# Optimization experiments

Measured on AMD Instinct MI355X. Metric: run time of the kernel, lower is better.

The kernel has to match this reference:

```python
import jax, jax.numpy as jnp
import numpy as np

EMBED_DIM = 256
NUM_HEADS = 8
HEAD_DIM = EMBED_DIM // NUM_HEADS


def setup_inputs() -> dict:
    key = jax.random.key(0)
    ks = jax.random.split(key, 16)
    B, N, E = 4, 2048, EMBED_DIM
    s = 1.0 / np.sqrt(E)
    inp = {
        "x": jax.random.normal(ks[0], (B, N, E), jnp.float32),
        "influence_matrix": jax.random.uniform(ks[1], (B, N, N), jnp.float32),
        "Wq": jax.random.normal(ks[2], (E, E), jnp.float32) * s,
        "Wk": jax.random.normal(ks[3], (E, E), jnp.float32) * s,
        "Wv": jax.random.normal(ks[4], (E, E), jnp.float32) * s,
        "Wo": jax.random.normal(ks[5], (E, E), jnp.float32) * s,
        "bo": jnp.zeros((E,), jnp.float32),
        "iw1": jnp.array(1.0, jnp.float32),
        "ib1": jnp.array(0.0, jnp.float32),
        "iw2": jnp.array(1.0, jnp.float32),
        "ib2": jnp.array(0.0, jnp.float32),
        "W1": jax.random.normal(ks[6], (E, E), jnp.float32) * s,
        "b1": jnp.zeros((E,), jnp.float32),
        "W2": jax.random.normal(ks[7], (E, E), jnp.float32) * s,
        "b2": jnp.zeros((E,), jnp.float32),
        "g1": jnp.ones((E,), jnp.float32),
        "beta1": jnp.zeros((E,), jnp.float32),
        "g2": jnp.ones((E,), jnp.float32),
        "beta2": jnp.zeros((E,), jnp.float32),
    }
    return inp


def _layer_norm(x, g, b, eps=1e-5):
    mu = jnp.mean(x, axis=-1, keepdims=True)
    var = jnp.var(x, axis=-1, keepdims=True)
    return (x - mu) * jax.lax.rsqrt(var + eps) * g + b


def _attention(x, infl, Wq, Wk, Wv, Wo, bo, iw1, ib1, iw2, ib2):
    B, N, E = x.shape
    H, D = NUM_HEADS, HEAD_DIM
    # torch nn.Linear: y = x @ W.T ; here W is stored as (E, E) used directly.
    q = (x @ Wq).reshape(B, N, H, D)
    k = (x @ Wk).reshape(B, N, H, D)
    v = (x @ Wv).reshape(B, N, H, D)
    scores = jnp.einsum("bqhd,bkhd->bhqk", q, k) / np.sqrt(D)  # [B,H,N,N]
    scores = scores + (iw1 * infl + ib1)[:, None, :, :]
    w = jax.nn.softmax(scores, axis=-1)
    w = w * (iw2 * infl + ib2)[:, None, :, :]
    out = jnp.einsum("bhqk,bkhd->bqhd", w, v).reshape(B, N, E)
    return out @ Wo + bo


def reference(x, influence_matrix, Wq, Wk, Wv, Wo, bo, iw1, ib1, iw2, ib2,
              W1, b1, W2, b2, g1, beta1, g2, beta2):
    h = _attention(_layer_norm(x, g1, beta1), influence_matrix,
                   Wq, Wk, Wv, Wo, bo, iw1, ib1, iw2, ib2) + x
    ffn = jax.nn.relu(_layer_norm(h, g2, beta2) @ W1 + b1) @ W2 + b2
    return ffn + h
```

## Files before the change

### kernel.cpp

```cpp
#include <hip/hip_runtime.h>
#include <hip/hip_bf16.h>

#define B_  4
#define N_  2048
#define E_  256
#define H_  8
#define D_  32
#define QT  32
#define KC  64
#define HPB 4
#define VTP 72
#define PP  72
#define IFP 68
#define LOG2E 1.4426950408889634f

typedef __attribute__((ext_vector_type(8))) short bfx8;
typedef __attribute__((ext_vector_type(4))) float fx4;

__device__ __forceinline__ unsigned short f2bf(float f) {
    unsigned int u = __float_as_uint(f);
    u += 0x7fffu + ((u >> 16) & 1u);
    return (unsigned short)(u >> 16);
}

__global__ __launch_bounds__(256) void prep_w(
    const float* Wa, const float* Wb, const float* Wc,
    const float* Wd, const float* We, const float* Wf,
    unsigned short* Oa, unsigned short* Ob, unsigned short* Oc,
    unsigned short* Od, unsigned short* Oe, unsigned short* Of)
{
    int z = blockIdx.z;
    const float* src = z == 0 ? Wa : z == 1 ? Wb : z == 2 ? Wc
                     : z == 3 ? Wd : z == 4 ? We : Wf;
    unsigned short* dst = z == 0 ? Oa : z == 1 ? Ob : z == 2 ? Oc
                        : z == 3 ? Od : z == 4 ? Oe : Of;
    __shared__ float t[32][33];
    int n0 = blockIdx.x * 32, k0 = blockIdx.y * 32;
    int tx = threadIdx.x & 31, ty = threadIdx.x >> 5;
#pragma unroll
    for (int i = 0; i < 4; i++)
        t[ty + i * 8][tx] = src[(k0 + ty + i * 8) * E_ + n0 + tx];
    __syncthreads();
#pragma unroll
    for (int i = 0; i < 4; i++)
        dst[(n0 + ty + i * 8) * E_ + k0 + tx] = f2bf(t[tx][ty + i * 8]);
}

__global__ __launch_bounds__(256) void ln_kernel(const float* __restrict__ x,
                                                 const float* __restrict__ g,
                                                 const float* __restrict__ be,
                                                 unsigned short* __restrict__ out)
{
    long row = blockIdx.x;
    int t = threadIdx.x;
    float v = x[row * E_ + t];
    float s = v, s2 = v * v;
#pragma unroll
    for (int off = 32; off; off >>= 1) {
        s  += __shfl_xor(s,  off, 64);
        s2 += __shfl_xor(s2, off, 64);
    }
    __shared__ float rs[4], rs2[4];
    int w = t >> 6;
    if ((t & 63) == 0) { rs[w] = s; rs2[w] = s2; }
    __syncthreads();
    s  = rs[0] + rs[1] + rs[2] + rs[3];
    s2 = rs2[0] + rs2[1] + rs2[2] + rs2[3];
    float mu  = s * (1.0f / E_);
    float var = s2 * (1.0f / E_) - mu * mu;
    float rstd = rsqrtf(var + 1e-5f);
    out[row * E_ + t] = f2bf((v - mu) * rstd * g[t] + be[t]);
}

__device__ __forceinline__ void gemm_core(
    const unsigned short* __restrict__ A,
    const unsigned short* __restrict__ Wt,
    const float* __restrict__ bias,
    const float* __restrict__ resid,
    void* __restrict__ Cv, int relu, int obf, int m0, int n0)
{
    __shared__ unsigned short As[64 * 264];
    __shared__ unsigned short Bs[64 * 264];
    int tid = threadIdx.x;

    {
        const unsigned short* Ab = A  + (long)m0 * E_;
        const unsigned short* Bb = Wt + (long)n0 * E_;
        bfx8 va[8], vb[8];
#pragma unroll
        for (int i = 0; i < 8; i++) va[i] = *(const bfx8*)&Ab[(i * 256 + tid) * 8];
#pragma unroll
        for (int i = 0; i < 8; i++) vb[i] = *(const bfx8*)&Bb[(i * 256 + tid) * 8];
#pragma unroll
        for (int i = 0; i < 8; i++) {
            int fo = i * 256 + tid;
            int row = fo >> 5, c8 = fo & 31;
            *(bfx8*)&As[row * 264 + c8 * 8] = va[i];
            *(bfx8*)&Bs[row * 264 + c8 * 8] = vb[i];
        }
    }
    __syncthreads();

    int lane = tid & 63, w = tid >> 6;
    int c = lane & 15, g = lane >> 4;
    int wm = (w >> 1) * 32, wn = (w & 1) * 32;
    fx4 acc[2][2] = {};

#pragma unroll
    for (int ks = 0; ks < 8; ks++) {
        bfx8 a0 = *(const bfx8*)&As[(wm + c)      * 264 + ks * 32 + g * 8];
        bfx8 a1 = *(const bfx8*)&As[(wm + 16 + c) * 264 + ks * 32 + g * 8];
        bfx8 b0 = *(const bfx8*)&Bs[(wn + c)      * 264 + ks * 32 + g * 8];
        bfx8 b1 = *(const bfx8*)&Bs[(wn + 16 + c) * 264 + ks * 32 + g * 8];
        acc[0][0] = __builtin_amdgcn_mfma_f32_16x16x32_bf16(a0, b0, acc[0][0], 0, 0, 0);
        acc[0][1] = __builtin_amdgcn_mfma_f32_16x16x32_bf16(a0, b1, acc[0][1], 0, 0, 0);
        acc[1][0] = __builtin_amdgcn_mfma_f32_16x16x32_bf16(a1, b0, acc[1][0], 0, 0, 0);
        acc[1][1] = __builtin_amdgcn_mfma_f32_16x16x32_bf16(a1, b1, acc[1][1], 0, 0, 0);
    }

#pragma unroll
    for (int fm = 0; fm < 2; fm++)
#pragma unroll
        for (int r = 0; r < 4; r++) {
            int m = m0 + wm + fm * 16 + g * 4 + r;
#pragma unroll
            for (int fn = 0; fn < 2; fn++) {
                int n = n0 + wn + fn * 16 + c;
                float o = acc[fm][fn][r];
                if (bias)  o += bias[n];
                if (relu)  o = fmaxf(o, 0.f);
                if (resid) o += resid[(long)m * E_ + n];
                if (obf) ((unsigned short*)Cv)[(long)m * E_ + n] = f2bf(o);
                else     ((float*)Cv)[(long)m * E_ + n] = o;
            }
        }
}

__global__ __launch_bounds__(256, 2) void gemm_mfma(
    const unsigned short* __restrict__ A,
    const unsigned short* __restrict__ Wt,
    const float* __restrict__ bias,
    const float* __restrict__ resid,
    void* __restrict__ Cv, int relu, int obf)
{
    gemm_core(A, Wt, bias, resid, Cv, relu, obf, blockIdx.x * 64, blockIdx.y * 64);
}

__global__ __launch_bounds__(256, 2) void gemm_qkv(
    const unsigned short* __restrict__ A,
    const unsigned short* __restrict__ Wq, unsigned short* __restrict__ qo,
    const unsigned short* __restrict__ Wk, unsigned short* __restrict__ ko,
    const unsigned short* __restrict__ Wv, unsigned short* __restrict__ vo)
{
    int z = blockIdx.z;
    const unsigned short* Wt = z == 0 ? Wq : z == 1 ? Wk : Wv;
    unsigned short*       Cv = z == 0 ? qo : z == 1 ? ko : vo;
    gemm_core(A, Wt, nullptr, nullptr, Cv, 0, 1, blockIdx.x * 64, blockIdx.y * 64);
}

__global__ __launch_bounds__(256, 2) void attn_mfma(
    const unsigned short* __restrict__ q,
    const unsigned short* __restrict__ k,
    const unsigned short* __restrict__ v,
    const float* __restrict__ infl,
    const float* __restrict__ iw1p, const float* __restrict__ ib1p,
    const float* __restrict__ iw2p, const float* __restrict__ ib2p,
    unsigned short* __restrict__ out)
{
    const int bx  = blockIdx.x;
    const int xcd = bx & 7;
    const int b   = xcd >> 1;
    const int hg  = (xcd & 1) * HPB;
    const int q0  = (bx >> 3) * QT;
    const int tid = threadIdx.x;
    const int h    = tid >> 6;
    const int head = hg + h;
    const int lane = tid & 63;
    const int c = lane & 15, g = lane >> 4, g4 = g * 4;

    const float iw1e = iw1p[0] * LOG2E, ib1e = ib1p[0] * LOG2E;
    const float iw2 = iw2p[0], ib2 = ib2p[0];
    const float scale2 = 0.17677669529663687f * LOG2E;
    const float cadd = ib1e - 16.0f * LOG2E;

    __shared__ unsigned short vt_lds[HPB][D_][VTP];
    __shared__ unsigned short p_lds[HPB][QT][PP];
    __shared__ unsigned short infl_lds[2][QT][IFP];

    bfx8 qf0 = *(const bfx8*)&q[((long)(b * N_ + q0 +      c)) * E_ + head * D_ + g * 8];
    bfx8 qf1 = *(const bfx8*)&q[((long)(b * N_ + q0 + 16 + c)) * E_ + head * D_ + g * 8];

    const unsigned short* kbase = &k[((long)(b * N_) + c) * E_ + head * D_ + g * 8];
    const int p2 = lane & 31, dh = (lane >> 5) * 16;
    const unsigned short* vbase = &v[((long)(b * N_) + 2 * p2) * E_ + head * D_ + dh];
    unsigned int* vtw = (unsigned int*)&vt_lds[h][0][0];

    const int irow = tid >> 3, icol = (tid & 7) * 8;
    const float* ibase = &infl[((long)(b * N_ + q0 + irow)) * N_ + icol];

    fx4 o00 = {0,0,0,0}, o01 = {0,0,0,0}, o10 = {0,0,0,0}, o11 = {0,0,0,0};
    float l0 = 0.f, l1 = 0.f;
    const fx4 zero = {0,0,0,0};
    fx4 st[2][4];

    float4 i00 = *(const float4*)&ibase[0];
    float4 i01 = *(const float4*)&ibase[4];
    float4 fA0 = *(const float4*)&ibase[KC];
    float4 fA1 = *(const float4*)&ibase[KC + 4];
    bfx8 nk0 = *(const bfx8*)(kbase +  0L * E_);
    bfx8 nk1 = *(const bfx8*)(kbase + 16L * E_);
    bfx8 nk2 = *(const bfx8*)(kbase + 32L * E_);
    bfx8 nk3 = *(const bfx8*)(kbase + 48L * E_);
    bfx8 nva0 = *(const bfx8*)(vbase);
    bfx8 nva1 = *(const bfx8*)(vbase + 8);
    bfx8 nvb0 = *(const bfx8*)(vbase + E_);
    bfx8 nvb1 = *(const bfx8*)(vbase + E_ + 8);
    {
        unsigned int w0 = (unsigned int)f2bf(i00.x) | ((unsigned int)f2bf(i00.y) << 16);
        unsigned int w1 = (unsigned int)f2bf(i00.z) | ((unsigned int)f2bf(i00.w) << 16);
        unsigned int w2 = (unsigned int)f2bf(i01.x) | ((unsigned int)f2bf(i01.y) << 16);
        unsigned int w3 = (unsigned int)f2bf(i01.z) | ((unsigned int)f2bf(i01.w) << 16);
        *(uint2*)&infl_lds[0][irow][icol]     = make_uint2(w0, w1);
        *(uint2*)&infl_lds[0][irow][icol + 4] = make_uint2(w2, w3);
    }
    __syncthreads();
    __builtin_amdgcn_s_setprio(1);
    st[0][0] = __builtin_amdgcn_mfma_f32_16x16x32_bf16(nk0, qf0, zero, 0, 0, 0);
    st[1][0] = __builtin_amdgcn_mfma_f32_16x16x32_bf16(nk0, qf1, zero, 0, 0, 0);
    st[0][1] = __builtin_amdgcn_mfma_f32_16x16x32_bf16(nk1, qf0, zero, 0, 0, 0);
    st[1][1] = __builtin_amdgcn_mfma_f32_16x16x32_bf16(nk1, qf1, zero, 0, 0, 0);
    st[0][2] = __builtin_amdgcn_mfma_f32_16x16x32_bf16(nk2, qf0, zero, 0, 0, 0);
    st[1][2] = __builtin_amdgcn_mfma_f32_16x16x32_bf16(nk2, qf1, zero, 0, 0, 0);
    st[0][3] = __builtin_amdgcn_mfma_f32_16x16x32_bf16(nk3, qf0, zero, 0, 0, 0);
    st[1][3] = __builtin_amdgcn_mfma_f32_16x16x32_bf16(nk3, qf1, zero, 0, 0, 0);
    __builtin_amdgcn_s_setprio(0);
    {
#pragma unroll
        for (int i = 0; i < 8; i++) {
            unsigned int val = (unsigned int)(unsigned short)nva0[i] |
                               ((unsigned int)(unsigned short)nvb0[i] << 16);
            vtw[(dh + i) * (VTP / 2) + p2] = val;
        }
#pragma unroll
        for (int i = 0; i < 8; i++) {
            unsigned int val = (unsigned int)(unsigned short)nva1[i] |
                               ((unsigned int)(unsigned short)nvb1[i] << 16);
            vtw[(dh + 8 + i) * (VTP / 2) + p2] = val;
        }
    }

    for (int kk = 0; kk < N_; kk += KC) {
        const int cur = (kk >> 6) & 1, nxt = cur ^ 1;
        const int kn  = (kk +     KC) & (N_ - 1);
        const int kn2 = (kk + 2 * KC) & (N_ - 1);

        const unsigned short* nvs = vbase + (long)kn * E_;
        nva0 = *(const bfx8*)(nvs);
        nva1 = *(const bfx8*)(nvs + 8);
        nvb0 = *(const bfx8*)(nvs + E_);
        nvb1 = *(const bfx8*)(nvs + E_ + 8);
        nk0 = *(const bfx8*)(kbase + (long)(kn +  0) * E_);
        nk1 = *(const bfx8*)(kbase + (long)(kn + 16) * E_);
        nk2 = *(const bfx8*)(kbase + (long)(kn + 32) * E_);
        nk3 = *(const bfx8*)(kbase + (long)(kn + 48) * E_);
        float4 fN0 = *(const float4*)&ibase[kn2];
        float4 fN1 = *(const float4*)&ibase[kn2 + 4];

        {
            unsigned int w0 = (unsigned int)f2bf(fA0.x) | ((unsigned int)f2bf(fA0.y) << 16);
            unsigned int w1 = (unsigned int)f2bf(fA0.z) | ((unsigned int)f2bf(fA0.w) << 16);
            unsigned int w2 = (unsigned int)f2bf(fA1.x) | ((unsigned int)f2bf(fA1.y) << 16);
            unsigned int w3 = (unsigned int)f2bf(fA1.z) | ((unsigned int)f2bf(fA1.w) << 16);
            *(uint2*)&infl_lds[nxt][irow][icol]     = make_uint2(w0, w1);
            *(uint2*)&infl_lds[nxt][irow][icol + 4] = make_uint2(w2, w3);
        }

#pragma unroll
        for (int qs = 0; qs < 2; qs++) {
#pragma unroll
            for (int t = 0; t < 4; t++) {
                uint2 iw = *(const uint2*)&infl_lds[cur][qs * 16 + c][t * 16 + g4];
                float fr[4];
                fr[0] = __uint_as_float(iw.x << 16);
                fr[1] = __uint_as_float(iw.x & 0xffff0000u);
                fr[2] = __uint_as_float(iw.y << 16);
                fr[3] = __uint_as_float(iw.y & 0xffff0000u);
                float pr[4];
#pragma unroll
                for (int r = 0; r < 4; r++) {
                    float s = fmaf(st[qs][t][r], scale2, fmaf(fr[r], iw1e, cadd));
                    float p = __builtin_amdgcn_exp2f(s);
                    if (qs == 0) l0 += p; else l1 += p;
                    pr[r] = p * fmaf(iw2, fr[r], ib2);
                }
                unsigned int lo = (unsigned int)f2bf(pr[0]) | ((unsigned int)f2bf(pr[1]) << 16);
                unsigned int hi = (unsigned int)f2bf(pr[2]) | ((unsigned int)f2bf(pr[3]) << 16);
                *(uint2*)&p_lds[h][qs * 16 + c][t * 16 + g4] = make_uint2(lo, hi);
            }
        }

        __builtin_amdgcn_s_setprio(1);
#pragma unroll
        for (int kh = 0; kh < 2; kh++) {
            bfx8 vf0 = *(const bfx8*)&vt_lds[h][c][g * 8 + kh * 32];
            bfx8 vf1 = *(const bfx8*)&vt_lds[h][16 + c][g * 8 + kh * 32];
            bfx8 pf0 = *(const bfx8*)&p_lds[h][c][g * 8 + kh * 32];
            bfx8 pf1 = *(const bfx8*)&p_lds[h][16 + c][g * 8 + kh * 32];
            o00 = __builtin_amdgcn_mfma_f32_16x16x32_bf16(pf0, vf0, o00, 0, 0, 0);
            o01 = __builtin_amdgcn_mfma_f32_16x16x32_bf16(pf0, vf1, o01, 0, 0, 0);
            o10 = __builtin_amdgcn_mfma_f32_16x16x32_bf16(pf1, vf0, o10, 0, 0, 0);
            o11 = __builtin_amdgcn_mfma_f32_16x16x32_bf16(pf1, vf1, o11, 0, 0, 0);
        }
        __builtin_amdgcn_s_setprio(0);

        __syncthreads();

        if (kk != N_ - KC) {
            __builtin_amdgcn_s_setprio(1);
            st[0][0] = __builtin_amdgcn_mfma_f32_16x16x32_bf16(nk0, qf0, zero, 0, 0, 0);
            st[1][0] = __builtin_amdgcn_mfma_f32_16x16x32_bf16(nk0, qf1, zero, 0, 0, 0);
            st[0][1] = __builtin_amdgcn_mfma_f32_16x16x32_bf16(nk1, qf0, zero, 0, 0, 0);
            st[1][1] = __builtin_amdgcn_mfma_f32_16x16x32_bf16(nk1, qf1, zero, 0, 0, 0);
            st[0][2] = __builtin_amdgcn_mfma_f32_16x16x32_bf16(nk2, qf0, zero, 0, 0, 0);
            st[1][2] = __builtin_amdgcn_mfma_f32_16x16x32_bf16(nk2, qf1, zero, 0, 0, 0);
            st[0][3] = __builtin_amdgcn_mfma_f32_16x16x32_bf16(nk3, qf0, zero, 0, 0, 0);
            st[1][3] = __builtin_amdgcn_mfma_f32_16x16x32_bf16(nk3, qf1, zero, 0, 0, 0);
            __builtin_amdgcn_s_setprio(0);
#pragma unroll
            for (int i = 0; i < 8; i++) {
                unsigned int val = (unsigned int)(unsigned short)nva0[i] |
                                   ((unsigned int)(unsigned short)nvb0[i] << 16);
                vtw[(dh + i) * (VTP / 2) + p2] = val;
            }
#pragma unroll
            for (int i = 0; i < 8; i++) {
                unsigned int val = (unsigned int)(unsigned short)nva1[i] |
                                   ((unsigned int)(unsigned short)nvb1[i] << 16);
                vtw[(dh + 8 + i) * (VTP / 2) + p2] = val;
            }
        }
        fA0 = fN0; fA1 = fN1;
    }

    float l0r = l0;
    l0r += __shfl_xor(l0r, 16); l0r += __shfl_xor(l0r, 32);
    float l1r = l1;
    l1r += __shfl_xor(l1r, 16); l1r += __shfl_xor(l1r, 32);
#pragma unroll
    for (int r = 0; r < 4; r++) {
        int src = (lane & 48) | (g4 + r);
        float inv0 = 1.0f / __shfl(l0r, src, 64);
        float inv1 = 1.0f / __shfl(l1r, src, 64);
        long row0 = ((long)(b * N_ + q0 +      g4 + r)) * E_ + head * D_;
        long row1 = ((long)(b * N_ + q0 + 16 + g4 + r)) * E_ + head * D_;
        out[row0 + c]      = f2bf(o00[r] * inv0);
        out[row0 + 16 + c] = f2bf(o01[r] * inv0);
        out[row1 + c]      = f2bf(o10[r] * inv1);
        out[row1 + 16 + c] = f2bf(o11[r] * inv1);
    }
}

extern "C" void kernel_launch(void* const* d_in, const int* in_sizes, int n_in,
                              void* d_out, int out_size, void* d_ws, size_t ws_size,
                              hipStream_t stream)
{
    (void)in_sizes; (void)n_in; (void)out_size; (void)ws_size;
    const float* x    = (const float*)d_in[0];
    const float* infl = (const float*)d_in[1];
    const float* Wq   = (const float*)d_in[2];
    const float* Wk   = (const float*)d_in[3];
    const float* Wv   = (const float*)d_in[4];
    const float* Wo   = (const float*)d_in[5];
    const float* bo   = (const float*)d_in[6];
    const float* iw1  = (const float*)d_in[7];
    const float* ib1  = (const float*)d_in[8];
    const float* iw2  = (const float*)d_in[9];
    const float* ib2  = (const float*)d_in[10];
    const float* W1   = (const float*)d_in[11];
    const float* b1   = (const float*)d_in[12];
    const float* W2   = (const float*)d_in[13];
    const float* b2   = (const float*)d_in[14];
    const float* g1   = (const float*)d_in[15];
    const float* be1  = (const float*)d_in[16];
    const float* g2   = (const float*)d_in[17];
    const float* be2  = (const float*)d_in[18];

    char* base = (char*)d_ws;
    float*          hb  = (float*)base;
    unsigned short* lnb = (unsigned short*)(base + (8  << 20));
    unsigned short* qb  = (unsigned short*)(base + (12 << 20));
    unsigned short* kb  = (unsigned short*)(base + (16 << 20));
    unsigned short* vb  = (unsigned short*)(base + (20 << 20));
    unsigned short* wqt = (unsigned short*)(base + (24 << 20));
    unsigned short* wkt = wqt + 65536;
    unsigned short* wvt = wkt + 65536;
    unsigned short* wot = wvt + 65536;
    unsigned short* w1t = wot + 65536;
    unsigned short* w2t = w1t + 65536;

    dim3 gemm_grid(128, 4);

    prep_w<<<dim3(8, 8, 6), 256, 0, stream>>>(Wq, Wk, Wv, Wo, W1, W2,
                                              wqt, wkt, wvt, wot, w1t, w2t);
    ln_kernel<<<B_ * N_, 256, 0, stream>>>(x, g1, be1, lnb);
    gemm_qkv<<<dim3(128, 4, 3), 256, 0, stream>>>(lnb, wqt, qb, wkt, kb, wvt, vb);
    attn_mfma<<<B_ * (N_ / QT) * 2, 256, 0, stream>>>(qb, kb, vb, infl,
                                                      iw1, ib1, iw2, ib2, lnb);
    gemm_mfma<<<gemm_grid, 256, 0, stream>>>(lnb, wot, bo, x, hb, 0, 0);
    ln_kernel<<<B_ * N_, 256, 0, stream>>>(hb, g2, be2, lnb);
    gemm_mfma<<<gemm_grid, 256, 0, stream>>>(lnb, w1t, b1, nullptr, qb, 1, 1);
    gemm_mfma<<<gemm_grid, 256, 0, stream>>>(qb, w2t, b2, hb, (float*)d_out, 0, 0);
}
```

Measured before the change: 149.1 us.

## Produce V transposed from QKV GEMM and keep influence tile in fp32 LDS

```diff
diff --git a/kernel.cpp b/kernel.cpp
--- a/kernel.cpp
+++ b/kernel.cpp
@@ -11,7 +11,7 @@
 #define HPB 4
 #define VTP 72
 #define PP  72
-#define IFP 68
+#define IFPF 68
 #define LOG2E 1.4426950408889634f
 
 typedef __attribute__((ext_vector_type(8))) short bfx8;
@@ -77,7 +77,7 @@
     const unsigned short* __restrict__ Wt,
     const float* __restrict__ bias,
     const float* __restrict__ resid,
-    void* __restrict__ Cv, int relu, int obf, int m0, int n0)
+    void* __restrict__ Cv, int relu, int obf, int m0, int n0, int ldC)
 {
     __shared__ unsigned short As[64 * 264];
     __shared__ unsigned short Bs[64 * 264];
@@ -129,9 +129,9 @@
                 float o = acc[fm][fn][r];
                 if (bias)  o += bias[n];
                 if (relu)  o = fmaxf(o, 0.f);
-                if (resid) o += resid[(long)m * E_ + n];
-                if (obf) ((unsigned short*)Cv)[(long)m * E_ + n] = f2bf(o);
-                else     ((float*)Cv)[(long)m * E_ + n] = o;
+                if (resid) o += resid[(long)m * ldC + n];
+                if (obf) ((unsigned short*)Cv)[(long)m * ldC + n] = f2bf(o);
+                else     ((float*)Cv)[(long)m * ldC + n] = o;
             }
         }
 }
@@ -143,25 +143,33 @@
     const float* __restrict__ resid,
     void* __restrict__ Cv, int relu, int obf)
 {
-    gemm_core(A, Wt, bias, resid, Cv, relu, obf, blockIdx.x * 64, blockIdx.y * 64);
+    gemm_core(A, Wt, bias, resid, Cv, relu, obf,
+              blockIdx.x * 64, blockIdx.y * 64, E_);
 }
 
 __global__ __launch_bounds__(256, 2) void gemm_qkv(
     const unsigned short* __restrict__ A,
     const unsigned short* __restrict__ Wq, unsigned short* __restrict__ qo,
     const unsigned short* __restrict__ Wk, unsigned short* __restrict__ ko,
-    const unsigned short* __restrict__ Wv, unsigned short* __restrict__ vo)
+    const unsigned short* __restrict__ Wv, unsigned short* __restrict__ vto)
 {
     int z = blockIdx.z;
-    const unsigned short* Wt = z == 0 ? Wq : z == 1 ? Wk : Wv;
-    unsigned short*       Cv = z == 0 ? qo : z == 1 ? ko : vo;
-    gemm_core(A, Wt, nullptr, nullptr, Cv, 0, 1, blockIdx.x * 64, blockIdx.y * 64);
+    if (z == 2) {
+        gemm_core(Wv, A, nullptr, nullptr, vto, 0, 1,
+                  blockIdx.y * 64, blockIdx.x * 64, B_ * N_);
+    } else {
+        const unsigned short* Wt = z == 0 ? Wq : Wk;
+        unsigned short*       Cv = z == 0 ? qo : Wk ? ko : ko;
+        Cv = z == 0 ? qo : ko;
+        gemm_core(A, Wt, nullptr, nullptr, Cv, 0, 1,
+                  blockIdx.x * 64, blockIdx.y * 64, E_);
+    }
 }
 
 __global__ __launch_bounds__(256, 2) void attn_mfma(
     const unsigned short* __restrict__ q,
     const unsigned short* __restrict__ k,
-    const unsigned short* __restrict__ v,
+    const unsigned short* __restrict__ vt,
     const float* __restrict__ infl,
     const float* __restrict__ iw1p, const float* __restrict__ ib1p,
     const float* __restrict__ iw2p, const float* __restrict__ ib2p,
@@ -185,15 +193,15 @@
 
     __shared__ unsigned short vt_lds[HPB][D_][VTP];
     __shared__ unsigned short p_lds[HPB][QT][PP];
-    __shared__ unsigned short infl_lds[2][QT][IFP];
+    __shared__ float infl_lds[2][QT][IFPF];
 
     bfx8 qf0 = *(const bfx8*)&q[((long)(b * N_ + q0 +      c)) * E_ + head * D_ + g * 8];
     bfx8 qf1 = *(const bfx8*)&q[((long)(b * N_ + q0 + 16 + c)) * E_ + head * D_ + g * 8];
 
     const unsigned short* kbase = &k[((long)(b * N_) + c) * E_ + head * D_ + g * 8];
-    const int p2 = lane & 31, dh = (lane >> 5) * 16;
-    const unsigned short* vbase = &v[((long)(b * N_) + 2 * p2) * E_ + head * D_ + dh];
-    unsigned int* vtw = (unsigned int*)&vt_lds[h][0][0];
+    const long MT = (long)B_ * N_;
+    const int vrow = lane >> 3, vcol = (lane & 7) * 8;
+    const unsigned short* vtg = &vt[((long)(head * D_ + vrow)) * MT + b * N_ + vcol];
 
     const int irow = tid >> 3, icol = (tid & 7) * 8;
     const float* ibase = &infl[((long)(b * N_ + q0 + irow)) * N_ + icol];
@@ -211,17 +219,13 @@
     bfx8 nk1 = *(const bfx8*)(kbase + 16L * E_);
     bfx8 nk2 = *(const bfx8*)(kbase + 32L * E_);
     bfx8 nk3 = *(const bfx8*)(kbase + 48L * E_);
-    bfx8 nva0 = *(const bfx8*)(vbase);
-    bfx8 nva1 = *(const bfx8*)(vbase + 8);
-    bfx8 nvb0 = *(const bfx8*)(vbase + E_);
-    bfx8 nvb1 = *(const bfx8*)(vbase + E_ + 8);
+    bfx8 nv0 = *(const bfx8*)(vtg +  0L * MT);
+    bfx8 nv1 = *(const bfx8*)(vtg +  8L * MT);
+    bfx8 nv2 = *(const bfx8*)(vtg + 16L * MT);
+    bfx8 nv3 = *(const bfx8*)(vtg + 24L * MT);
     {
-        unsigned int w0 = (unsigned int)f2bf(i00.x) | ((unsigned int)f2bf(i00.y) << 16);
-        unsigned int w1 = (unsigned int)f2bf(i00.z) | ((unsigned int)f2bf(i00.w) << 16);
-        unsigned int w2 = (unsigned int)f2bf(i01.x) | ((unsigned int)f2bf(i01.y) << 16);
-        unsigned int w3 = (unsigned int)f2bf(i01.z) | ((unsigned int)f2bf(i01.w) << 16);
-        *(uint2*)&infl_lds[0][irow][icol]     = make_uint2(w0, w1);
-        *(uint2*)&infl_lds[0][irow][icol + 4] = make_uint2(w2, w3);
+        *(float4*)&infl_lds[0][irow][icol]     = i00;
+        *(float4*)&infl_lds[0][irow][icol + 4] = i01;
     }
     __syncthreads();
     __builtin_amdgcn_s_setprio(1);
@@ -235,18 +239,10 @@
     st[1][3] = __builtin_amdgcn_mfma_f32_16x16x32_bf16(nk3, qf1, zero, 0, 0, 0);
     __builtin_amdgcn_s_setprio(0);
     {
-#pragma unroll
-        for (int i = 0; i < 8; i++) {
-            unsigned int val = (unsigned int)(unsigned short)nva0[i] |
-                               ((unsigned int)(unsigned short)nvb0[i] << 16);
-            vtw[(dh + i) * (VTP / 2) + p2] = val;
-        }
-#pragma unroll
-        for (int i = 0; i < 8; i++) {
-            unsigned int val = (unsigned int)(unsigned short)nva1[i] |
-                               ((unsigned int)(unsigned short)nvb1[i] << 16);
-            vtw[(dh + 8 + i) * (VTP / 2) + p2] = val;
-        }
+        *(bfx8*)&vt_lds[h][vrow     ][vcol] = nv0;
+        *(bfx8*)&vt_lds[h][vrow +  8][vcol] = nv1;
+        *(bfx8*)&vt_lds[h][vrow + 16][vcol] = nv2;
+        *(bfx8*)&vt_lds[h][vrow + 24][vcol] = nv3;
     }
 
     for (int kk = 0; kk < N_; kk += KC) {
@@ -254,11 +250,10 @@
         const int kn  = (kk +     KC) & (N_ - 1);
         const int kn2 = (kk + 2 * KC) & (N_ - 1);
 
-        const unsigned short* nvs = vbase + (long)kn * E_;
-        nva0 = *(const bfx8*)(nvs);
-        nva1 = *(const bfx8*)(nvs + 8);
-        nvb0 = *(const bfx8*)(nvs + E_);
-        nvb1 = *(const bfx8*)(nvs + E_ + 8);
+        nv0 = *(const bfx8*)(vtg +  0L * MT + kn);
+        nv1 = *(const bfx8*)(vtg +  8L * MT + kn);
+        nv2 = *(const bfx8*)(vtg + 16L * MT + kn);
+        nv3 = *(const bfx8*)(vtg + 24L * MT + kn);
         nk0 = *(const bfx8*)(kbase + (long)(kn +  0) * E_);
         nk1 = *(const bfx8*)(kbase + (long)(kn + 16) * E_);
         nk2 = *(const bfx8*)(kbase + (long)(kn + 32) * E_);
@@ -266,25 +261,15 @@
         float4 fN0 = *(const float4*)&ibase[kn2];
         float4 fN1 = *(const float4*)&ibase[kn2 + 4];
 
-        {
-            unsigned int w0 = (unsigned int)f2bf(fA0.x) | ((unsigned int)f2bf(fA0.y) << 16);
-            unsigned int w1 = (unsigned int)f2bf(fA0.z) | ((unsigned int)f2bf(fA0.w) << 16);
-            unsigned int w2 = (unsigned int)f2bf(fA1.x) | ((unsigned int)f2bf(fA1.y) << 16);
-            unsigned int w3 = (unsigned int)f2bf(fA1.z) | ((unsigned int)f2bf(fA1.w) << 16);
-            *(uint2*)&infl_lds[nxt][irow][icol]     = make_uint2(w0, w1);
-            *(uint2*)&infl_lds[nxt][irow][icol + 4] = make_uint2(w2, w3);
-        }
+        *(float4*)&infl_lds[nxt][irow][icol]     = fA0;
+        *(float4*)&infl_lds[nxt][irow][icol + 4] = fA1;
 
 #pragma unroll
         for (int qs = 0; qs < 2; qs++) {
 #pragma unroll
             for (int t = 0; t < 4; t++) {
-                uint2 iw = *(const uint2*)&infl_lds[cur][qs * 16 + c][t * 16 + g4];
-                float fr[4];
-                fr[0] = __uint_as_float(iw.x << 16);
-                fr[1] = __uint_as_float(iw.x & 0xffff0000u);
-                fr[2] = __uint_as_float(iw.y << 16);
-                fr[3] = __uint_as_float(iw.y & 0xffff0000u);
+                float4 fr4 = *(const float4*)&infl_lds[cur][qs * 16 + c][t * 16 + g4];
+                float fr[4] = {fr4.x, fr4.y, fr4.z, fr4.w};
                 float pr[4];
 #pragma unroll
                 for (int r = 0; r < 4; r++) {
@@ -326,18 +311,10 @@
             st[0][3] = __builtin_amdgcn_mfma_f32_16x16x32_bf16(nk3, qf0, zero, 0, 0, 0);
             st[1][3] = __builtin_amdgcn_mfma_f32_16x16x32_bf16(nk3, qf1, zero, 0, 0, 0);
             __builtin_amdgcn_s_setprio(0);
-#pragma unroll
-            for (int i = 0; i < 8; i++) {
-                unsigned int val = (unsigned int)(unsigned short)nva0[i] |
-                                   ((unsigned int)(unsigned short)nvb0[i] << 16);
-                vtw[(dh + i) * (VTP / 2) + p2] = val;
-            }
-#pragma unroll
-            for (int i = 0; i < 8; i++) {
-                unsigned int val = (unsigned int)(unsigned short)nva1[i] |
-                                   ((unsigned int)(unsigned short)nvb1[i] << 16);
-                vtw[(dh + 8 + i) * (VTP / 2) + p2] = val;
-            }
+            *(bfx8*)&vt_lds[h][vrow     ][vcol] = nv0;
+            *(bfx8*)&vt_lds[h][vrow +  8][vcol] = nv1;
+            *(bfx8*)&vt_lds[h][vrow + 16][vcol] = nv2;
+            *(bfx8*)&vt_lds[h][vrow + 24][vcol] = nv3;
         }
         fA0 = fN0; fA1 = fN1;
     }
@@ -390,7 +367,7 @@
     unsigned short* lnb = (unsigned short*)(base + (8  << 20));
     unsigned short* qb  = (unsigned short*)(base + (12 << 20));
     unsigned short* kb  = (unsigned short*)(base + (16 << 20));
-    unsigned short* vb  = (unsigned short*)(base + (20 << 20));
+    unsigned short* vtb = (unsigned short*)(base + (20 << 20));
     unsigned short* wqt = (unsigned short*)(base + (24 << 20));
     unsigned short* wkt = wqt + 65536;
     unsigned short* wvt = wkt + 65536;
@@ -403,8 +380,8 @@
     prep_w<<<dim3(8, 8, 6), 256, 0, stream>>>(Wq, Wk, Wv, Wo, W1, W2,
                                               wqt, wkt, wvt, wot, w1t, w2t);
     ln_kernel<<<B_ * N_, 256, 0, stream>>>(x, g1, be1, lnb);
-    gemm_qkv<<<dim3(128, 4, 3), 256, 0, stream>>>(lnb, wqt, qb, wkt, kb, wvt, vb);
-    attn_mfma<<<B_ * (N_ / QT) * 2, 256, 0, stream>>>(qb, kb, vb, infl,
+    gemm_qkv<<<dim3(128, 4, 3), 256, 0, stream>>>(lnb, wqt, qb, wkt, kb, wvt, vtb);
+    attn_mfma<<<B_ * (N_ / QT) * 2, 256, 0, stream>>>(qb, kb, vtb, infl,
                                                       iw1, ib1, iw2, ib2, lnb);
     gemm_mfma<<<gemm_grid, 256, 0, stream>>>(lnb, wot, bo, x, hb, 0, 0);
     ln_kernel<<<B_ * N_, 256, 0, stream>>>(hb, g2, be2, lnb);
```

New measurement: 137.0 us. 8.1% less time.
